# Performance work log

Hardware: AMD Instinct MI355X
Metric: run time of the kernel (lower is better)

Reference implementation:

```python
import jax, jax.numpy as jnp
import numpy as np

N = 512          # Cartesian grid size (nRead)
C = 16           # n_coils
K = 262144       # n non-uniform k-space samples (~512 spokes x 512 readouts)


def setup_inputs() -> dict:
    key = jax.random.key(0)
    ks = jax.random.split(key, 6)
    x_real = jax.random.normal(ks[0], (C, K), jnp.float32)
    x_imag = jax.random.normal(ks[1], (C, K), jnp.float32)
    csm_real = jax.random.normal(ks[2], (C, N, N), jnp.float32)
    csm_imag = jax.random.normal(ks[3], (C, N, N), jnp.float32)
    # normalized k-space coordinates in [-0.5, 0.5)
    traj = jax.random.uniform(ks[4], (K, 2), jnp.float32, -0.5, 0.5)
    # density compensation weights (positive)
    dcf = jax.random.uniform(ks[5], (K,), jnp.float32)
    return dict(x_real=x_real, x_imag=x_imag, csm_real=csm_real,
                csm_imag=csm_imag, traj=traj, dcf=dcf)


def reference(x_real, x_imag, csm_real, csm_imag, traj, dcf):
    # Adjoint gridding NUFFT with density compensation + coil-sensitivity combine.
    # 1) density-compensate the multicoil non-Cartesian samples
    x = (x_real + 1j * x_imag) * dcf                      # [C, K] complex64
    # 2) grid (scatter-add) onto the Cartesian k-space grid (nearest-cell gridding)
    t = jax.lax.stop_gradient(traj)
    idx = jnp.round((t + 0.5) * N).astype(jnp.int32) % N  # [K, 2]
    iy, ix = idx[:, 0], idx[:, 1]
    grid = jnp.zeros((C, N, N), jnp.complex64).at[:, iy, ix].add(x)
    # 3) centered inverse FFT to image space (adjoint of DFT, scaled by N^2)
    img = jnp.fft.fftshift(
        jnp.fft.ifft2(jnp.fft.ifftshift(grid, axes=(-2, -1)), axes=(-2, -1)),
        axes=(-2, -1)) * (N * N)                          # [C, N, N]
    # 4) coil combine with conjugate sensitivity maps
    csm = csm_real + 1j * csm_imag
    out = jnp.sum(jnp.conj(csm) * img, axis=0)            # [N, N] complex64
    # return real/imag stacked, with batch dim (mimics numpy2tensor add_batch_dim)
    return jnp.stack([out.real, out.imag])[None]          # [1, 2, N, N]
```

## Files before the change

### kernel.cpp

```cpp
#include <hip/hip_runtime.h>
#include <math.h>

#define N 512
#define NN (N * N)
#define C 16
#define K 262144
#define LOG2N 9

#define SK(e) ((e) + ((e) >> 4))
#define LROW 544

__device__ __forceinline__ float4 f4add(float4 a, float4 b) {
    return make_float4(a.x + b.x, a.y + b.y, a.z + b.z, a.w + b.w);
}
__device__ __forceinline__ float4 f4sub(float4 a, float4 b) {
    return make_float4(a.x - b.x, a.y - b.y, a.z - b.z, a.w - b.w);
}
__device__ __forceinline__ float4 cmulf4(float4 a, float c, float s) {
    return make_float4(c * a.x - s * a.y, c * a.y + s * a.x,
                       c * a.z - s * a.w, c * a.w + s * a.z);
}
__device__ __forceinline__ float4 cmuli(float4 a) {
    return make_float4(-a.y, a.x, -a.w, a.z);
}

__device__ __forceinline__ void rad8(float4* stripe, int p0, int h, float th1) {
    float s1, c1, s2, c2, s3, c3;
    __sincosf(th1, &s1, &c1);
    __sincosf(0.5f * th1, &s2, &c2);
    __sincosf(0.25f * th1, &s3, &c3);
    const float r2 = 0.70710678118654752f;
    float c3r = r2 * (c3 - s3), s3r = r2 * (c3 + s3);
    float4 x0 = stripe[SK(p0)];
    float4 x1 = stripe[SK(p0 + h)];
    float4 x2 = stripe[SK(p0 + 2 * h)];
    float4 x3 = stripe[SK(p0 + 3 * h)];
    float4 x4 = stripe[SK(p0 + 4 * h)];
    float4 x5 = stripe[SK(p0 + 5 * h)];
    float4 x6 = stripe[SK(p0 + 6 * h)];
    float4 x7 = stripe[SK(p0 + 7 * h)];
    float4 t;
    t = cmulf4(x1, c1, s1); float4 y0 = f4add(x0, t), y1 = f4sub(x0, t);
    t = cmulf4(x3, c1, s1); float4 y2 = f4add(x2, t), y3 = f4sub(x2, t);
    t = cmulf4(x5, c1, s1); float4 y4 = f4add(x4, t), y5 = f4sub(x4, t);
    t = cmulf4(x7, c1, s1); float4 y6 = f4add(x6, t), y7 = f4sub(x6, t);
    t = cmulf4(y2, c2, s2);        float4 z0 = f4add(y0, t), z2 = f4sub(y0, t);
    t = cmuli(cmulf4(y3, c2, s2)); float4 z1 = f4add(y1, t), z3 = f4sub(y1, t);
    t = cmulf4(y6, c2, s2);        float4 z4 = f4add(y4, t), z6 = f4sub(y4, t);
    t = cmuli(cmulf4(y7, c2, s2)); float4 z5 = f4add(y5, t), z7 = f4sub(y5, t);
    float4 w0 = cmulf4(z4, c3, s3);
    float4 w1 = cmulf4(z5, c3r, s3r);
    float4 w2 = cmuli(cmulf4(z6, c3, s3));
    float4 w3 = cmuli(cmulf4(z7, c3r, s3r));
    stripe[SK(p0)]         = f4add(z0, w0);
    stripe[SK(p0 + 4 * h)] = f4sub(z0, w0);
    stripe[SK(p0 + h)]     = f4add(z1, w1);
    stripe[SK(p0 + 5 * h)] = f4sub(z1, w1);
    stripe[SK(p0 + 2 * h)] = f4add(z2, w2);
    stripe[SK(p0 + 6 * h)] = f4sub(z2, w2);
    stripe[SK(p0 + 3 * h)] = f4add(z3, w3);
    stripe[SK(p0 + 7 * h)] = f4sub(z3, w3);
}

__device__ __forceinline__ void fft512_wave(float4* stripe, int l) {
    rad8(stripe, l * 8, 1, 0.0f);
    asm volatile("s_waitcnt lgkmcnt(0)" ::: "memory");
    rad8(stripe, (l >> 3) * 64 + (l & 7), 8,
         6.283185307179586f * (float)(l & 7) * (1.0f / 16.0f));
    asm volatile("s_waitcnt lgkmcnt(0)" ::: "memory");
    rad8(stripe, l, 64,
         6.283185307179586f * (float)l * (1.0f / 128.0f));
    asm volatile("s_waitcnt lgkmcnt(0)" ::: "memory");
}

__global__ __launch_bounds__(256) void prep_hist_kernel(const float4* __restrict__ traj2,
                                                        int* __restrict__ count) {
    int k2 = blockIdx.x * 256 + threadIdx.x;
    float4 t2 = traj2[k2];
    int iy0 = __float2int_rn((t2.x + 0.5f) * (float)N) & (N - 1);
    int ix0 = __float2int_rn((t2.y + 0.5f) * (float)N) & (N - 1);
    int iy1 = __float2int_rn((t2.z + 0.5f) * (float)N) & (N - 1);
    int ix1 = __float2int_rn((t2.w + 0.5f) * (float)N) & (N - 1);
    atomicAdd(&count[iy0 * N + ix0], 1);
    atomicAdd(&count[iy1 * N + ix1], 1);
}

__global__ __launch_bounds__(256) void scan_reduce_kernel(const int* __restrict__ count,
                                                          int* __restrict__ bsum) {
    __shared__ int sd[256];
    int t = threadIdx.x;
    const int4* c4 = (const int4*)count;
    int4 v = c4[blockIdx.x * 256 + t];
    sd[t] = v.x + v.y + v.z + v.w;
    __syncthreads();
    for (int d = 128; d > 0; d >>= 1) {
        if (t < d) sd[t] += sd[t + d];
        __syncthreads();
    }
    if (t == 0) bsum[blockIdx.x] = sd[0];
}

__global__ __launch_bounds__(256) void scan_final2_kernel(const int* __restrict__ count,
                                                          const int* __restrict__ bsum,
                                                          int* __restrict__ offs,
                                                          int* __restrict__ cursor) {
    __shared__ int sb[256];
    __shared__ int sd[256];
    int t = threadIdx.x;
    int b = blockIdx.x;
    int vb = bsum[t];
    sb[t] = vb;
    __syncthreads();
    for (int d = 1; d < 256; d <<= 1) {
        int tmp = (t >= d) ? sb[t - d] : 0;
        __syncthreads();
        sb[t] += tmp;
        __syncthreads();
    }
    int4 c4 = ((const int4*)count)[b * 256 + t];
    int s = c4.x + c4.y + c4.z + c4.w;
    sd[t] = s;
    __syncthreads();
    for (int d = 1; d < 256; d <<= 1) {
        int tmp = (t >= d) ? sd[t - d] : 0;
        __syncthreads();
        sd[t] += tmp;
        __syncthreads();
    }
    int bexc = sb[b] - bsum[b];
    int base = bexc + sd[t] - s;
    int4 o;
    o.x = base;
    o.y = base + c4.x;
    o.z = base + c4.x + c4.y;
    o.w = base + c4.x + c4.y + c4.z;
    ((int4*)offs)[b * 256 + t] = o;
    ((int4*)cursor)[b * 256 + t] = o;
    if (b == 0 && t == 0) offs[NN] = K;
}

__global__ __launch_bounds__(256) void payload_kernel(const float* __restrict__ xr,
                                                      const float* __restrict__ xi,
                                                      const float2* __restrict__ traj,
                                                      const float* __restrict__ dcf,
                                                      int* __restrict__ cursor,
                                                      float2* __restrict__ pay) {
    __shared__ float tR[256][17];
    __shared__ float tI[256][17];
    __shared__ int   sp[256];
    __shared__ float sw[256];
    int t = threadIdx.x;
    int k0 = blockIdx.x * 256;
#pragma unroll
    for (int c = 0; c < C; ++c) {
        tR[t][c] = xr[(size_t)c * K + k0 + t];
        tI[t][c] = xi[(size_t)c * K + k0 + t];
    }
    float2 tr = traj[k0 + t];
    int iy = __float2int_rn((tr.x + 0.5f) * (float)N) & (N - 1);
    int ix = __float2int_rn((tr.y + 0.5f) * (float)N) & (N - 1);
    int cl = iy * N + ix;
    sp[t] = atomicAdd(&cursor[cl], 1);
    sw[t] = dcf[k0 + t] * (((iy + ix) & 1) ? -1.0f : 1.0f);
    __syncthreads();
    int sg = t >> 4, l = t & 15;
    for (int j = sg; j < 256; j += 16) {
        int pp = sp[j];
        float ww = sw[j];
        pay[(size_t)pp * 16 + l] = make_float2(tR[j][l] * ww, tI[j][l] * ww);
    }
}

__global__ __launch_bounds__(256) void build8_kernel(const int* __restrict__ offs,
                                                     const float4* __restrict__ pay4,
                                                     float2* __restrict__ grid) {
    __shared__ float4 lds[4][LROW];
    int bid = blockIdx.x;
    int h = bid & 1;
    int r = bid >> 1;
    int t = threadIdx.x;
    int w = t >> 6;
    int l = t & 63;
    int q = h * 4 + w;
    const int* ro = offs + r * N;

    int sv[8], ev[8];
#pragma unroll
    for (int it = 0; it < 8; ++it) {
        int col = l + (it << 6);
        sv[it] = ro[col];
        ev[it] = ro[col + 1];
    }
    float4 vv[8], vv2[8];
#pragma unroll
    for (int it = 0; it < 8; ++it) {
        vv[it] = make_float4(0.f, 0.f, 0.f, 0.f);
        if (sv[it] < ev[it]) vv[it] = pay4[(size_t)sv[it] * 8 + q];
    }
#pragma unroll
    for (int it = 0; it < 8; ++it) {
        vv2[it] = make_float4(0.f, 0.f, 0.f, 0.f);
        if (sv[it] + 1 < ev[it]) vv2[it] = pay4[(size_t)(sv[it] + 1) * 8 + q];
    }
#pragma unroll
    for (int it = 0; it < 8; ++it) {
        float4 acc = make_float4(vv[it].x + vv2[it].x, vv[it].y + vv2[it].y,
                                 vv[it].z + vv2[it].z, vv[it].w + vv2[it].w);
        for (int p = sv[it] + 2; p < ev[it]; ++p) {
            float4 v2 = pay4[(size_t)p * 8 + q];
            acc.x += v2.x; acc.y += v2.y; acc.z += v2.z; acc.w += v2.w;
        }
        int col = l + (it << 6);
        int bc = (int)(__brev((unsigned)col) >> (32 - LOG2N));
        lds[w][SK(bc)] = acc;
    }
    asm volatile("s_waitcnt lgkmcnt(0)" ::: "memory");

    fft512_wave(&lds[w][0], l);

    int c0 = q * 2;
    float2* g0 = grid + (size_t)c0 * NN + (size_t)r * N;
    float2* g1 = grid + (size_t)(c0 + 1) * NN + (size_t)r * N;
    for (int i = l; i < N; i += 64) {
        float4 v = lds[w][SK(i)];
        g0[i] = make_float2(v.x, v.y);
        g1[i] = make_float2(v.z, v.w);
    }
}

__global__ __launch_bounds__(512) void colfft_kernel(float2* __restrict__ grid) {
    __shared__ float4 lds[8][LROW];
    int blk = blockIdx.x;
    int c = blk >> 5;
    int cg = blk & 31;
    int t = threadIdx.x;
    int w = t >> 6;
    int l = t & 63;
    int colb = cg * 16 + w * 2;
    float2* gp = grid + (size_t)c * NN + colb;

#pragma unroll
    for (int j = 0; j < 8; ++j) {
        int row = l + (j << 6);
        float4 v = *(const float4*)(gp + (size_t)row * N);
        int br = (int)(__brev((unsigned)row) >> (32 - LOG2N));
        lds[w][SK(br)] = v;
    }
    asm volatile("s_waitcnt lgkmcnt(0)" ::: "memory");

    fft512_wave(&lds[w][0], l);

#pragma unroll
    for (int j = 0; j < 8; ++j) {
        int i = l + (j << 6);
        *(float4*)(gp + (size_t)i * N) = lds[w][SK(i)];
    }
}

__global__ __launch_bounds__(256) void combine_kernel(const float* __restrict__ csr,
                                                      const float* __restrict__ csi,
                                                      const float2* __restrict__ grid,
                                                      float* __restrict__ out) {
    int p2 = blockIdx.x * 256 + threadIdx.x;
    int pix = p2 * 2;
    int ny = pix >> LOG2N, nx = pix & (N - 1);
    float ar0 = 0.f, ai0 = 0.f, ar1 = 0.f, ai1 = 0.f;
#pragma unroll
    for (int c = 0; c < C; ++c) {
        float4 uv = ((const float4*)(grid + (size_t)c * NN))[p2];
        float2 a = ((const float2*)(csr + (size_t)c * NN))[p2];
        float2 b = ((const float2*)(csi + (size_t)c * NN))[p2];
        ar0 += a.x * uv.x + b.x * uv.y;
        ai0 += a.x * uv.y - b.x * uv.x;
        ar1 += a.y * uv.z + b.y * uv.w;
        ai1 += a.y * uv.w - b.y * uv.z;
    }
    float s0 = ((ny + nx) & 1) ? -1.f : 1.f;
    float s1 = -s0;
    ((float2*)out)[p2] = make_float2(s0 * ar0, s1 * ar1);
    ((float2*)(out + NN))[p2] = make_float2(s0 * ai0, s1 * ai1);
}

extern "C" void kernel_launch(void* const* d_in, const int* in_sizes, int n_in,
                              void* d_out, int out_size, void* d_ws, size_t ws_size,
                              hipStream_t stream) {
    const float* x_real   = (const float*)d_in[0];
    const float* x_imag   = (const float*)d_in[1];
    const float* csm_real = (const float*)d_in[2];
    const float* csm_imag = (const float*)d_in[3];
    const float2* traj    = (const float2*)d_in[4];
    const float* dcf      = (const float*)d_in[5];
    float* out = (float*)d_out;

    char* ws = (char*)d_ws;
    size_t o = 0;
    float* grid  = (float*)(ws + o); o += (size_t)C * NN * 2 * sizeof(float);
    int*   count = (int*)(ws + o);   o += (size_t)NN * sizeof(int);
    int*   offs  = (int*)(ws + o);   o += ((size_t)NN + 4) * sizeof(int);
    int*   cursor= (int*)(ws + o);   o += (size_t)NN * sizeof(int);
    float2* pay  = (float2*)(ws + o); o += (size_t)K * 16 * sizeof(float2);
    int*   bsum  = (int*)(ws + o);   o += 256 * sizeof(int);

    (void)hipMemsetAsync(count, 0, (size_t)NN * sizeof(int), stream);

    prep_hist_kernel<<<K / 512, 256, 0, stream>>>((const float4*)traj, count);
    scan_reduce_kernel<<<256, 256, 0, stream>>>(count, bsum);
    scan_final2_kernel<<<256, 256, 0, stream>>>(count, bsum, offs, cursor);
    payload_kernel<<<K / 256, 256, 0, stream>>>(x_real, x_imag, traj, dcf, cursor, pay);
    build8_kernel<<<N * 2, 256, 0, stream>>>(offs, (const float4*)pay, (float2*)grid);
    colfft_kernel<<<C * 32, 512, 0, stream>>>((float2*)grid);
    combine_kernel<<<NN / 512, 256, 0, stream>>>(csm_real, csm_imag, (float2*)grid, out);
}
```

Baseline: 196.7 us.

## Fuse scan kernels, widen row-build blocks, and coalesce column FFT loads

```diff
diff --git a/kernel.cpp b/kernel.cpp
--- a/kernel.cpp
+++ b/kernel.cpp
@@ -8,7 +8,7 @@
 #define LOG2N 9
 
 #define SK(e) ((e) + ((e) >> 4))
-#define LROW 544
+#define LROW 545
 
 __device__ __forceinline__ float4 f4add(float4 a, float4 b) {
     return make_float4(a.x + b.x, a.y + b.y, a.z + b.z, a.w + b.w);
@@ -85,39 +85,15 @@
     atomicAdd(&count[iy1 * N + ix1], 1);
 }
 
-__global__ __launch_bounds__(256) void scan_reduce_kernel(const int* __restrict__ count,
-                                                          int* __restrict__ bsum) {
-    __shared__ int sd[256];
-    int t = threadIdx.x;
-    const int4* c4 = (const int4*)count;
-    int4 v = c4[blockIdx.x * 256 + t];
-    sd[t] = v.x + v.y + v.z + v.w;
-    __syncthreads();
-    for (int d = 128; d > 0; d >>= 1) {
-        if (t < d) sd[t] += sd[t + d];
-        __syncthreads();
-    }
-    if (t == 0) bsum[blockIdx.x] = sd[0];
-}
-
-__global__ __launch_bounds__(256) void scan_final2_kernel(const int* __restrict__ count,
-                                                          const int* __restrict__ bsum,
-                                                          int* __restrict__ offs,
-                                                          int* __restrict__ cursor) {
-    __shared__ int sb[256];
+__global__ __launch_bounds__(256) void scan_kernel(const int* __restrict__ count,
+                                                   int* __restrict__ offs,
+                                                   int* __restrict__ cursor) {
     __shared__ int sd[256];
     int t = threadIdx.x;
     int b = blockIdx.x;
-    int vb = bsum[t];
-    sb[t] = vb;
-    __syncthreads();
-    for (int d = 1; d < 256; d <<= 1) {
-        int tmp = (t >= d) ? sb[t - d] : 0;
-        __syncthreads();
-        sb[t] += tmp;
-        __syncthreads();
-    }
-    int4 c4 = ((const int4*)count)[b * 256 + t];
+    const int4* c4all = (const int4*)count;
+
+    int4 c4 = c4all[b * 256 + t];
     int s = c4.x + c4.y + c4.z + c4.w;
     sd[t] = s;
     __syncthreads();
@@ -127,8 +103,31 @@
         sd[t] += tmp;
         __syncthreads();
     }
-    int bexc = sb[b] - bsum[b];
-    int base = bexc + sd[t] - s;
+    int epre = sd[t] - s;
+
+    int lim = b * 256;
+    int p0 = 0, p1 = 0, p2 = 0, p3 = 0;
+    int i = t;
+    for (; i + 768 < lim; i += 1024) {
+        int4 a = c4all[i], bb = c4all[i + 256], cc = c4all[i + 512], dd = c4all[i + 768];
+        p0 += a.x + a.y + a.z + a.w;
+        p1 += bb.x + bb.y + bb.z + bb.w;
+        p2 += cc.x + cc.y + cc.z + cc.w;
+        p3 += dd.x + dd.y + dd.z + dd.w;
+    }
+    for (; i < lim; i += 256) {
+        int4 a = c4all[i];
+        p0 += a.x + a.y + a.z + a.w;
+    }
+    __syncthreads();
+    sd[t] = p0 + p1 + p2 + p3;
+    __syncthreads();
+    for (int d = 128; d > 0; d >>= 1) {
+        if (t < d) sd[t] += sd[t + d];
+        __syncthreads();
+    }
+    int base = sd[0] + epre;
+
     int4 o;
     o.x = base;
     o.y = base + c4.x;
@@ -171,17 +170,14 @@
     }
 }
 
-__global__ __launch_bounds__(256) void build8_kernel(const int* __restrict__ offs,
+__global__ __launch_bounds__(512) void build8_kernel(const int* __restrict__ offs,
                                                      const float4* __restrict__ pay4,
                                                      float2* __restrict__ grid) {
-    __shared__ float4 lds[4][LROW];
-    int bid = blockIdx.x;
-    int h = bid & 1;
-    int r = bid >> 1;
+    __shared__ float4 lds[8][LROW];
+    int r = blockIdx.x;
     int t = threadIdx.x;
     int w = t >> 6;
     int l = t & 63;
-    int q = h * 4 + w;
     const int* ro = offs + r * N;
 
     int sv[8], ev[8];
@@ -195,19 +191,19 @@
 #pragma unroll
     for (int it = 0; it < 8; ++it) {
         vv[it] = make_float4(0.f, 0.f, 0.f, 0.f);
-        if (sv[it] < ev[it]) vv[it] = pay4[(size_t)sv[it] * 8 + q];
+        if (sv[it] < ev[it]) vv[it] = pay4[(size_t)sv[it] * 8 + w];
     }
 #pragma unroll
     for (int it = 0; it < 8; ++it) {
         vv2[it] = make_float4(0.f, 0.f, 0.f, 0.f);
-        if (sv[it] + 1 < ev[it]) vv2[it] = pay4[(size_t)(sv[it] + 1) * 8 + q];
+        if (sv[it] + 1 < ev[it]) vv2[it] = pay4[(size_t)(sv[it] + 1) * 8 + w];
     }
 #pragma unroll
     for (int it = 0; it < 8; ++it) {
         float4 acc = make_float4(vv[it].x + vv2[it].x, vv[it].y + vv2[it].y,
                                  vv[it].z + vv2[it].z, vv[it].w + vv2[it].w);
         for (int p = sv[it] + 2; p < ev[it]; ++p) {
-            float4 v2 = pay4[(size_t)p * 8 + q];
+            float4 v2 = pay4[(size_t)p * 8 + w];
             acc.x += v2.x; acc.y += v2.y; acc.z += v2.z; acc.w += v2.w;
         }
         int col = l + (it << 6);
@@ -218,7 +214,7 @@
 
     fft512_wave(&lds[w][0], l);
 
-    int c0 = q * 2;
+    int c0 = w * 2;
     float2* g0 = grid + (size_t)c0 * NN + (size_t)r * N;
     float2* g1 = grid + (size_t)(c0 + 1) * NN + (size_t)r * N;
     for (int i = l; i < N; i += 64) {
@@ -236,24 +232,26 @@
     int t = threadIdx.x;
     int w = t >> 6;
     int l = t & 63;
-    int colb = cg * 16 + w * 2;
-    float2* gp = grid + (size_t)c * NN + colb;
+    float2* gb = grid + (size_t)c * NN + cg * 16;
+    int cp = t & 7;
+    int r0 = t >> 3;
 
 #pragma unroll
     for (int j = 0; j < 8; ++j) {
-        int row = l + (j << 6);
-        float4 v = *(const float4*)(gp + (size_t)row * N);
+        int row = r0 + (j << 6);
+        float4 v = ((const float4*)(gb + (size_t)row * N))[cp];
         int br = (int)(__brev((unsigned)row) >> (32 - LOG2N));
-        lds[w][SK(br)] = v;
-    }
-    asm volatile("s_waitcnt lgkmcnt(0)" ::: "memory");
+        lds[cp][SK(br)] = v;
+    }
+    __syncthreads();
 
     fft512_wave(&lds[w][0], l);
+    __syncthreads();
 
 #pragma unroll
     for (int j = 0; j < 8; ++j) {
-        int i = l + (j << 6);
-        *(float4*)(gp + (size_t)i * N) = lds[w][SK(i)];
+        int row = r0 + (j << 6);
+        ((float4*)(gb + (size_t)row * N))[cp] = lds[cp][SK(row)];
     }
 }
 
@@ -299,15 +297,13 @@
     int*   offs  = (int*)(ws + o);   o += ((size_t)NN + 4) * sizeof(int);
     int*   cursor= (int*)(ws + o);   o += (size_t)NN * sizeof(int);
     float2* pay  = (float2*)(ws + o); o += (size_t)K * 16 * sizeof(float2);
-    int*   bsum  = (int*)(ws + o);   o += 256 * sizeof(int);
 
     (void)hipMemsetAsync(count, 0, (size_t)NN * sizeof(int), stream);
 
     prep_hist_kernel<<<K / 512, 256, 0, stream>>>((const float4*)traj, count);
-    scan_reduce_kernel<<<256, 256, 0, stream>>>(count, bsum);
-    scan_final2_kernel<<<256, 256, 0, stream>>>(count, bsum, offs, cursor);
+    scan_kernel<<<256, 256, 0, stream>>>(count, offs, cursor);
     payload_kernel<<<K / 256, 256, 0, stream>>>(x_real, x_imag, traj, dcf, cursor, pay);
-    build8_kernel<<<N * 2, 256, 0, stream>>>(offs, (const float4*)pay, (float2*)grid);
+    build8_kernel<<<N, 512, 0, stream>>>(offs, (const float4*)pay, (float2*)grid);
     colfft_kernel<<<C * 32, 512, 0, stream>>>((float2*)grid);
     combine_kernel<<<NN / 512, 256, 0, stream>>>(csm_real, csm_imag, (float2*)grid, out);
 }
```

New measurement: 193.7 us (median of 2 runs). No clear change (-1.5%).
